# Optimization experiments

Measured on AMD Instinct MI355X. Metric: run time of the kernel, lower is better.

The kernel has to match this reference:

```python
import jax, jax.numpy as jnp
import numpy as np

B, TV, F, H, V, NSTEPS = 64, 40, 2048, 1024, 32000, 30


def setup_inputs() -> dict:
    key = jax.random.key(0)
    ks = jax.random.split(key, 26)
    s = 0.02
    return {
        "batch_size": B,
        "action_feat": jax.random.normal(ks[0], (B, TV, F), jnp.float32),
        "imagenet_feat": jax.random.normal(ks[1], (B, TV, F), jnp.float32),
        "video_mask": jnp.ones((B, TV), jnp.float32),
        "captions": jax.random.randint(ks[2], (B, NSTEPS + 1), 0, V),
        "caption_mask": jnp.ones((B, NSTEPS + 1), jnp.float32),
        "enc_img_W": jax.random.normal(ks[3], (F, H), jnp.float32) * s,
        "enc_img_b": jax.random.normal(ks[4], (H,), jnp.float32) * s,
        "enc_mean_W": jax.random.normal(ks[5], (F, H), jnp.float32) * s,
        "enc_mean_b": jax.random.normal(ks[6], (H,), jnp.float32) * s,
        "att_w": jax.random.normal(ks[7], (H,), jnp.float32) * s,
        "att_Wa": jax.random.normal(ks[8], (H, H), jnp.float32) * s,
        "att_Ua": jax.random.normal(ks[9], (H, H), jnp.float32) * s,
        "att_ba": jax.random.normal(ks[10], (H,), jnp.float32) * s,
        "Wemb": jax.random.normal(ks[11], (V, H), jnp.float32) * s,
        "embed_word_W": jax.random.normal(ks[12], (H, V), jnp.float32) * s,
        "embed_word_b": jax.random.normal(ks[13], (V,), jnp.float32) * s,
        "lstm1_Wih": jax.random.normal(ks[14], (4 * H, 2 * H), jnp.float32) * s,
        "lstm1_Whh": jax.random.normal(ks[15], (4 * H, H), jnp.float32) * s,
        "lstm1_bih": jax.random.normal(ks[16], (4 * H,), jnp.float32) * s,
        "lstm1_bhh": jax.random.normal(ks[17], (4 * H,), jnp.float32) * s,
        "lstm2_Wih": jax.random.normal(ks[18], (4 * H, H), jnp.float32) * s,
        "lstm2_Whh": jax.random.normal(ks[19], (4 * H, H), jnp.float32) * s,
        "lstm2_bih": jax.random.normal(ks[20], (4 * H,), jnp.float32) * s,
        "lstm2_bhh": jax.random.normal(ks[21], (4 * H,), jnp.float32) * s,
    }


def _lstm_cell(x, h, c, Wih, Whh, bih, bhh):
    # PyTorch LSTMCell: gates in order (i, f, g, o)
    g = x @ Wih.T + bih + h @ Whh.T + bhh
    i, f, gg, o = jnp.split(g, 4, axis=-1)
    c_new = jax.nn.sigmoid(f) * c + jax.nn.sigmoid(i) * jnp.tanh(gg)
    h_new = jax.nn.sigmoid(o) * jnp.tanh(c_new)
    return h_new, c_new


def reference(batch_size, action_feat, imagenet_feat, video_mask, captions,
              caption_mask, enc_img_W, enc_img_b, enc_mean_W, enc_mean_b,
              att_w, att_Wa, att_Ua, att_ba, Wemb, embed_word_W, embed_word_b,
              lstm1_Wih, lstm1_Whh, lstm1_bih, lstm1_bhh,
              lstm2_Wih, lstm2_Whh, lstm2_bih, lstm2_bhh):
    bsz = action_feat.shape[0]
    # source code overwrites cat(action, imagenet) with action_feat alone
    video_feat = action_feat @ enc_img_W + enc_img_b          # [B, Tv, H]
    vid_emb = jnp.transpose(video_feat, (1, 0, 2))            # [Tv, B, H]
    feat_mean = jnp.mean(action_feat, axis=1)                 # [B, F]
    feat_mean = feat_mean @ enc_mean_W + enc_mean_b           # [B, H]

    image_part = jnp.einsum('tbh,hk->tbk', vid_emb, att_Ua) + att_ba  # [Tv,B,H]
    vm = video_mask.T                                         # [Tv, B]

    n = captions.shape[1] - 1
    emb_seq = jnp.transpose(Wemb[captions[:, :n]], (1, 0, 2))  # [n, B, H]
    tgts = captions[:, 1:n + 1].T                              # [n, B]
    masks = caption_mask[:, 1:n + 1].T                         # [n, B]

    zeros_h = jnp.zeros((bsz, vid_emb.shape[-1]), jnp.float32)

    def step(carry, xs):
        h1, c1, h2, c2, h_prev, loss = carry
        emb_t, tgt_t, mask_t = xs
        # Bahdanau attention with custom masked softmax
        e = jnp.tanh(h_prev @ att_Wa + image_part)             # [Tv, B, H]
        e = jnp.einsum('tbh,h->tb', e, att_w)                  # [Tv, B]
        e_max = jnp.max(e, axis=0)                             # [B]
        e_hat = vm * jnp.exp(e - e_max)                        # [Tv, B]
        denom = jnp.sum(e_hat, axis=0)
        denom = denom + (denom == 0.0).astype(jnp.float32) + 1e-9
        e_div = e_hat / denom                                  # [Tv, B]
        atten = jnp.einsum('tb,tbh->bh', e_div, vid_emb)       # [B, H]

        x1 = jnp.concatenate([emb_t, atten], axis=1)           # [B, 2H]
        h1, c1 = _lstm_cell(x1, h1, c1, lstm1_Wih, lstm1_Whh, lstm1_bih, lstm1_bhh)
        h2, c2 = _lstm_cell(h1, h2, c2, lstm2_Wih, lstm2_Whh, lstm2_bih, lstm2_bhh)

        logits = h2 @ embed_word_W + embed_word_b              # [B, V]
        logp = jax.nn.log_softmax(logits, axis=-1)
        ce_mean = -jnp.mean(jnp.take_along_axis(logp, tgt_t[:, None], axis=1)[:, 0])
        # original: scalar mean-CE broadcast over mask, summed, / batch_size
        loss = loss + ce_mean * jnp.sum(mask_t) / bsz
        return (h1, c1, h2, c2, h2, loss), None

    init = (feat_mean, zeros_h, zeros_h, zeros_h, feat_mean, jnp.float32(0.0))
    (h1, c1, h2, c2, h_prev, total_loss), _ = jax.lax.scan(
        step, init, (emb_seq, tgts, masks))
    return total_loss
```

## Files before the change

### kernel.cpp

```cpp
#include <hip/hip_runtime.h>
#include <stdint.h>

constexpr int kB   = 64;
constexpr int kTV  = 40;
constexpr int kF   = 2048;
constexpr int kH   = 1024;
constexpr int kV   = 32000;
constexpr int kNS  = 30;
constexpr int kCAP = 31;

typedef __attribute__((ext_vector_type(8))) short bf16x8;
typedef __attribute__((ext_vector_type(4))) float f32x4;
typedef unsigned short us;

__device__ __forceinline__ float sigm(float x) { return 1.f / (1.f + __expf(-x)); }
__device__ __forceinline__ float tanh_fast(float x) {
    float e = __expf(2.f * x);
    return 1.f - 2.f / (e + 1.f);
}
__device__ __forceinline__ us f2bf(float x) {
    unsigned u = __float_as_uint(x);
    return (us)((u + 0x7fffu + ((u >> 16) & 1u)) >> 16);
}
__device__ __forceinline__ float bf2f(us u) {
    return __uint_as_float((unsigned)u << 16);
}

__device__ __forceinline__ void gl16(const us* g, us* lds) {
    __builtin_amdgcn_global_load_lds(
        (const __attribute__((address_space(1))) unsigned int*)(g),
        (__attribute__((address_space(3))) unsigned int*)(lds), 16, 0, 0);
}

template <int N>
__device__ __forceinline__ void waitv() {
    asm volatile("s_waitcnt vmcnt(%0)" :: "n"(N) : "memory");
}
__device__ __forceinline__ void barrier_raw() {
    __builtin_amdgcn_s_barrier();
    asm volatile("" ::: "memory");
}

__device__ __forceinline__ void store_packedA(us* base, int row, int col, us v) {
    int kt = col >> 5, kc = col & 31, ms = row >> 4;
    int l = (row & 15) + (((kc >> 2) & 3) << 4);
    int j = (kc & 3) + ((kc >> 4) << 2);
    base[((((size_t)kt * 4 + ms) * 64 + l) << 3) + j] = v;
}

template <int NSPW, int KT>
__device__ __forceinline__ void mfma_kloop(
    const us* __restrict__ Ap, const us* __restrict__ Bp,
    us* Asm, us* Bsm, int w, int l, f32x4 acc[4][NSPW])
{
    constexpr int BSTEP = 2048 * NSPW;
    constexpr int LPT = 1 + NSPW;
    auto stage = [&](int t, int slot) {
        gl16(Ap + (size_t)t * 2048 + w * 512 + l * 8, Asm + slot * 2048 + w * 512);
#pragma unroll
        for (int i = 0; i < NSPW; ++i)
            gl16(Bp + (size_t)t * BSTEP + (w * NSPW + i) * 512 + l * 8,
                 Bsm + slot * BSTEP + (w * NSPW + i) * 512);
    };
    stage(0, 0);
    if (1 < KT) stage(1, 1);
#pragma unroll 1
    for (int t = 0; t < KT; ++t) {
        int slot = t % 3;
        if (t + 1 < KT) waitv<LPT>();
        else waitv<0>();
        barrier_raw();
        if (t + 2 < KT) stage(t + 2, (t + 2) % 3);
        bf16x8 bfr[NSPW], afr[4];
#pragma unroll
        for (int i = 0; i < NSPW; ++i)
            bfr[i] = *(const bf16x8*)(Bsm + slot * BSTEP + ((w * NSPW + i) * 64 + l) * 8);
#pragma unroll
        for (int ms = 0; ms < 4; ++ms)
            afr[ms] = *(const bf16x8*)(Asm + slot * 2048 + (ms * 64 + l) * 8);
#pragma unroll
        for (int ms = 0; ms < 4; ++ms)
#pragma unroll
            for (int i = 0; i < NSPW; ++i)
                acc[ms][i] = __builtin_amdgcn_mfma_f32_16x16x32_bf16(
                    afr[ms], bfr[i], acc[ms][i], 0, 0, 0);
        __builtin_amdgcn_sched_barrier(0);
    }
}

__global__ __launch_bounds__(256) void prep_mean(
    const float* __restrict__ af, float* __restrict__ fm,
    const float* __restrict__ bih1, const float* __restrict__ bhh1,
    const float* __restrict__ bih2, const float* __restrict__ bhh2,
    const float* __restrict__ capmask,
    float* __restrict__ bsum1, float* __restrict__ bsum2, float* __restrict__ msum)
{
    int tid = threadIdx.x;
    if (blockIdx.x < 64) {
        int b = blockIdx.x;
        const float* base = af + (size_t)b * kTV * kF;
        float a[8] = {};
        for (int t = 0; t < kTV; ++t) {
            const float* rp = base + (size_t)t * kF + tid * 8;
            float4 v0 = *(const float4*)rp;
            float4 v1 = *(const float4*)(rp + 4);
            a[0] += v0.x; a[1] += v0.y; a[2] += v0.z; a[3] += v0.w;
            a[4] += v1.x; a[5] += v1.y; a[6] += v1.z; a[7] += v1.w;
        }
        float* op = fm + (size_t)b * kF + tid * 8;
#pragma unroll
        for (int j = 0; j < 8; ++j) op[j] = a[j] * (1.f / kTV);
    } else {
        int g = (blockIdx.x - 64) * 256 + tid;
        if (g < 4096) bsum1[g] = bih1[g] + bhh1[g];
        else if (g < 8192) { int j = g - 4096; bsum2[j] = bih2[j] + bhh2[j]; }
        else if (g < 8192 + kNS) {
            int t = g - 8192;
            float s = 0.f;
            for (int b = 0; b < kB; ++b) s += capmask[b * kCAP + t + 1];
            msum[t] = s;
        }
    }
}

__global__ __launch_bounds__(256) void pack_rm(
    const float* __restrict__ p0, int ld0, int ksplit,
    const float* __restrict__ p1, int ld1,
    int NGRP, int GS, int HS, int KT,
    us* __restrict__ out)
{
    __shared__ us tile[16][136];
    int kb = blockIdx.x * 128;
    int grp = blockIdx.y;
    int row0 = (grp % NGRP) * GS + (grp / NGRP) * HS;
    int tid = threadIdx.x;
    int r = tid >> 5, c4 = (tid & 31) * 4;
#pragma unroll
    for (int pass = 0; pass < 2; ++pass) {
        int rr = r + pass * 8;
        int row = row0 + rr;
        int k = kb + c4;
        float4 v;
        if (k < ksplit) v = *(const float4*)(p0 + (size_t)row * ld0 + k);
        else            v = *(const float4*)(p1 + (size_t)row * ld1 + (k - ksplit));
        ushort4 o; o.x = f2bf(v.x); o.y = f2bf(v.y); o.z = f2bf(v.z); o.w = f2bf(v.w);
        *(ushort4*)&tile[rr][c4] = o;
    }
    __syncthreads();
    int ktl = tid >> 6, l = tid & 63, ul = l & 15, q = (l >> 4) & 3;
    __align__(16) us o2[8];
#pragma unroll
    for (int j = 0; j < 8; ++j) {
        int kc = (j & 3) + q * 4 + ((j >> 2) << 4);
        o2[j] = tile[ul][ktl * 32 + kc];
    }
    int kt = (kb >> 5) + ktl;
    size_t base = (((size_t)(grp / NGRP) * KT + kt) * NGRP + (grp % NGRP)) * 512;
    *(uint4*)(out + base + (size_t)l * 8) = *(const uint4*)o2;
}

__global__ __launch_bounds__(256) void pack_cm(const float* __restrict__ W,
                                               us* __restrict__ out)
{
    __shared__ us tile[32][136];
    int n0 = blockIdx.x * 128, k0 = blockIdx.y * 32;
    int tid = threadIdx.x;
    int r = tid >> 5, c4 = (tid & 31) * 4;
#pragma unroll
    for (int pass = 0; pass < 4; ++pass) {
        int rr = r + pass * 8;
        float4 v = *(const float4*)(W + (size_t)(k0 + rr) * kV + n0 + c4);
        ushort4 o; o.x = f2bf(v.x); o.y = f2bf(v.y); o.z = f2bf(v.z); o.w = f2bf(v.w);
        *(ushort4*)&tile[rr][c4] = o;
    }
    __syncthreads();
    int ns = tid >> 5, lp = (tid & 31) * 2;
    size_t base = (((size_t)blockIdx.x * 32 + blockIdx.y) * 8 + ns) * 512;
    __align__(16) us o2[16];
#pragma unroll
    for (int li = 0; li < 2; ++li) {
        int l = lp + li, ul = l & 15, q = (l >> 4) & 3;
#pragma unroll
        for (int j = 0; j < 8; ++j) {
            int kc = (j & 3) + q * 4 + ((j >> 2) << 4);
            o2[li * 8 + j] = tile[kc][ns * 16 + ul];
        }
    }
    *(uint4*)(out + base + lp * 8) = *(const uint4*)&o2[0];
    *(uint4*)(out + base + lp * 8 + 8) = *(const uint4*)&o2[8];
}

__global__ __launch_bounds__(256) void pack_sm4(
    const float* __restrict__ Wi, const float* __restrict__ Wm,
    const float* __restrict__ Wua, const float* __restrict__ Wa,
    us* __restrict__ oi, us* __restrict__ om,
    us* __restrict__ oua, us* __restrict__ oa)
{
    int bid = blockIdx.x;
    const float* W; us* out; int KT, rel;
    if (bid < 512)       { W = Wi;  out = oi;  KT = 64; rel = bid; }
    else if (bid < 1024) { W = Wm;  out = om;  KT = 64; rel = bid - 512; }
    else if (bid < 1280) { W = Wua; out = oua; KT = 32; rel = bid - 1024; }
    else                 { W = Wa;  out = oa;  KT = 32; rel = bid - 1280; }
    int bx = rel & 7, by = rel >> 3;
    __shared__ us tile[32][136];
    int n0 = bx * 128, k0 = by * 32;
    int tid = threadIdx.x;
    int r = tid >> 5, c4 = (tid & 31) * 4;
#pragma unroll
    for (int pass = 0; pass < 4; ++pass) {
        int rr = r + pass * 8;
        float4 v = *(const float4*)(W + (size_t)(k0 + rr) * 1024 + n0 + c4);
        ushort4 o; o.x = f2bf(v.x); o.y = f2bf(v.y); o.z = f2bf(v.z); o.w = f2bf(v.w);
        *(ushort4*)&tile[rr][c4] = o;
    }
    __syncthreads();
    int ns = tid >> 5, lp = (tid & 31) * 2;
    int nb64 = bx * 2 + (ns >> 2), ns4 = ns & 3;
    size_t base = (((size_t)nb64 * KT + by) * 4 + ns4) * 512;
    __align__(16) us o2[16];
#pragma unroll
    for (int li = 0; li < 2; ++li) {
        int l = lp + li, ul = l & 15, q = (l >> 4) & 3;
#pragma unroll
        for (int j = 0; j < 8; ++j) {
            int kc = (j & 3) + q * 4 + ((j >> 2) << 4);
            o2[li * 8 + j] = tile[kc][ns * 16 + ul];
        }
    }
    *(uint4*)(out + base + lp * 8) = *(const uint4*)&o2[0];
    *(uint4*)(out + base + lp * 8 + 8) = *(const uint4*)&o2[8];
}

__global__ __launch_bounds__(256) void pack_wae(const float* __restrict__ Wa,
                                                us* __restrict__ WaE)
{
    int nb = blockIdx.x >> 4, cb = blockIdx.x & 15;
    int tid = threadIdx.x;
    int ns = tid >> 6, l = tid & 63;
    int ul = l & 15, q = (l >> 4) & 3;
    int col = cb * 64 + ns * 16 + ul;
    __align__(16) us o[8];
#pragma unroll
    for (int j = 0; j < 4; ++j) {
        int k = (j & 3) + q * 4;
        o[j] = f2bf(Wa[(size_t)(nb * 16 + k) * kH + col]);
    }
    o[4] = 0; o[5] = 0; o[6] = 0; o[7] = 0;
    size_t base = (((size_t)(nb * 16 + cb)) * 4 + ns) * 512;
    *(uint4*)(WaE + base + (size_t)l * 8) = *(const uint4*)o;
}

__global__ __launch_bounds__(256) void pack_emb(
    const float* __restrict__ Wemb, const int* __restrict__ captions,
    us* __restrict__ embP)
{
    __shared__ us tile[16][136];
    int rel = blockIdx.x;
    int s = rel / 32, rem = rel % 32;
    int rg = rem & 3, kb8 = rem >> 2;
    int tid = threadIdx.x;
    int r = tid >> 5, c4 = (tid & 31) * 4;
#pragma unroll
    for (int pass = 0; pass < 2; ++pass) {
        int rr = r + pass * 8;
        int b = rg * 16 + rr;
        int word = captions[b * kCAP + s];
        float4 v = *(const float4*)(Wemb + (size_t)word * kH + kb8 * 128 + c4);
        ushort4 o; o.x = f2bf(v.x); o.y = f2bf(v.y); o.z = f2bf(v.z); o.w = f2bf(v.w);
        *(ushort4*)&tile[rr][c4] = o;
    }
    __syncthreads();
    int ktl = tid >> 6, l = tid & 63, ul = l & 15, q = (l >> 4) & 3;
    __align__(16) us o2[8];
#pragma unroll
    for (int j = 0; j < 8; ++j) {
        int kc = (j & 3) + q * 4 + ((j >> 2) << 4);
        o2[j] = tile[ul][ktl * 32 + kc];
    }
    int kt = kb8 * 4 + ktl;
    size_t base = (((size_t)s * 32 + kt) * 4 + rg) * 512;
    *(uint4*)(embP + base + (size_t)l * 8) = *(const uint4*)o2;
}

template <int KT>
__global__ __launch_bounds__(256) void enc_gemm(
    const us* __restrict__ Ap, const us* __restrict__ Bp,
    const float* __restrict__ bias, us* __restrict__ outF,
    us* __restrict__ outP)
{
    __shared__ us Asm[3][2048];
    __shared__ us Bsm[3][2048];
    int tid = threadIdx.x, w = tid >> 6, l = tid & 63;
    int nb = blockIdx.x, mb = blockIdx.y;
    f32x4 acc[4][1] = {};
    mfma_kloop<1, KT>(Ap + (size_t)mb * KT * 2048, Bp + (size_t)nb * KT * 2048,
                      &Asm[0][0], &Bsm[0][0], w, l, acc);
    int ul = l & 15, sg = l >> 4;
    int n = nb * 64 + w * 16 + ul;
    float bv = bias[n];
#pragma unroll
    for (int ms = 0; ms < 4; ++ms)
#pragma unroll
        for (int r = 0; r < 4; ++r) {
            int rl = ms * 16 + sg * 4 + r;
            int row = mb * 64 + rl;
            float v = acc[ms][0][r] + bv;
            outF[(size_t)row * kH + n] = f2bf(v);
            if (outP) store_packedA(outP + (size_t)mb * 65536, rl, n, f2bf(v));
        }
}

__global__ __launch_bounds__(256) void p3_gemm(
    const us* __restrict__ Ap, const us* __restrict__ Bp,
    const float* __restrict__ bias, us* __restrict__ xcat1p,
    us* __restrict__ h2hist0)
{
    __shared__ us Asm[3][2048];
    __shared__ us Bsm[3][2048];
    int tid = threadIdx.x, w = tid >> 6, l = tid & 63;
    int nb = blockIdx.x;
    f32x4 acc[4][1] = {};
    mfma_kloop<1, 64>(Ap, Bp + (size_t)nb * 64 * 2048, &Asm[0][0], &Bsm[0][0], w, l, acc);
    int ul = l & 15, sg = l >> 4;
    int n = nb * 64 + w * 16 + ul;
    float bv = bias[n];
#pragma unroll
    for (int ms = 0; ms < 4; ++ms)
#pragma unroll
        for (int r = 0; r < 4; ++r) {
            int row = ms * 16 + sg * 4 + r;
            us hb = f2bf(acc[ms][0][r] + bv);
            store_packedA(xcat1p, row, 1024 + n, hb);
            store_packedA(h2hist0, row, n, hb);
        }
}

__global__ __launch_bounds__(256) void gemb_gemm(
    const us* __restrict__ embP, const us* __restrict__ W1p,
    us* __restrict__ Gemb)
{
    __shared__ us Asm[3][2048];
    __shared__ us Bsm[3][2048];
    int rel = blockIdx.x;
    int s = rel >> 6, nb = rel & 63;
    int tid = threadIdx.x, w = tid >> 6, l = tid & 63;
    f32x4 acc[4][1] = {};
    mfma_kloop<1, 32>(embP + (size_t)s * 65536, W1p + (size_t)nb * 96 * 2048,
                      &Asm[0][0], &Bsm[0][0], w, l, acc);
    int ul = l & 15, sg = l >> 4;
    int n = nb * 64 + w * 16 + ul;
#pragma unroll
    for (int ms = 0; ms < 4; ++ms)
#pragma unroll
        for (int r = 0; r < 4; ++r) {
            int row = ms * 16 + sg * 4 + r;
            Gemb[((size_t)s * 64 + row) * 4096 + n] = f2bf(acc[ms][0][r]);
        }
}

__global__ __launch_bounds__(512) void hwa_gemm(
    const us* __restrict__ h2p, const us* __restrict__ WaP,
    float* __restrict__ hw)
{
    __shared__ __align__(16) char smem[49152];
    float* rsum = (float*)smem;
    int tid = threadIdx.x, w = tid >> 6, l = tid & 63, nb = blockIdx.x;
    int h = w >> 2, w4 = w & 3;
    us* Asm = (us*)(smem + h * 24576);
    us* Bsm = Asm + 6144;
    f32x4 acc[4][1] = {};
    mfma_kloop<1, 16>(h2p + (size_t)h * 16 * 2048,
                      WaP + (size_t)nb * 32 * 2048 + (size_t)h * 16 * 2048,
                      Asm, Bsm, w4, l, acc);
    int ul = l & 15, sg = l >> 4;
    __syncthreads();
    if (h == 1) {
#pragma unroll
        for (int ms = 0; ms < 4; ++ms)
#pragma unroll
            for (int r = 0; r < 4; ++r)
                rsum[((w4 * 64) + ms * 16 + sg * 4 + r) * 17 + ul] = acc[ms][0][r];
    }
    __syncthreads();
    if (h == 0) {
        int n = nb * 64 + w4 * 16 + ul;
#pragma unroll
        for (int ms = 0; ms < 4; ++ms)
#pragma unroll
            for (int r = 0; r < 4; ++r) {
                int row = ms * 16 + sg * 4 + r;
                hw[(size_t)row * kH + n] =
                    acc[ms][0][r] + rsum[((w4 * 64) + row) * 17 + ul];
            }
    }
}

__global__ __launch_bounds__(256) void attn_fused(
    const float* __restrict__ hw0, const us* __restrict__ hwP,
    const us* __restrict__ imgp, const float* __restrict__ attw,
    const us* __restrict__ vf, const float* __restrict__ vmask,
    us* __restrict__ xcat1p)
{
    __shared__ float hwv[kH];
    __shared__ float es[48];
    int b = blockIdx.x, tid = threadIdx.x;
    if (hw0) {
        for (int i = tid; i < kH; i += 256) hwv[i] = hw0[(size_t)b * kH + i];
    } else {
        int c4 = tid * 4;
        float a0 = 0.f, a1 = 0.f, a2 = 0.f, a3 = 0.f;
        for (int nb = 0; nb < 64; ++nb) {
            ushort4 v = *(const ushort4*)(hwP + ((size_t)nb * 64 + b) * 1024 + c4);
            a0 += bf2f(v.x); a1 += bf2f(v.y); a2 += bf2f(v.z); a3 += bf2f(v.w);
        }
        hwv[c4 + 0] = a0; hwv[c4 + 1] = a1; hwv[c4 + 2] = a2; hwv[c4 + 3] = a3;
    }
    __syncthreads();
    int w = tid >> 6, l = tid & 63;
    for (int t = w; t < kTV; t += 4) {
        const us* ip = imgp + ((size_t)b * kTV + t) * kH;
        float p = 0.f;
#pragma unroll
        for (int hh = 0; hh < 16; ++hh) {
            int h = hh * 64 + l;
            p += tanh_fast(hwv[h] + bf2f(ip[h])) * attw[h];
        }
        for (int off = 32; off; off >>= 1) p += __shfl_down(p, off);
        if (l == 0) es[t] = p;
    }
    __syncthreads();
    float mx = -1e30f;
    for (int t = 0; t < kTV; ++t) mx = fmaxf(mx, es[t]);
    const float* vm = vmask + b * kTV;
    float den = 0.f;
    for (int t = 0; t < kTV; ++t) den += vm[t] * __expf(es[t] - mx);
    den = den + (den == 0.f ? 1.f : 0.f) + 1e-9f;
    int h0 = tid * 4;
    float a0 = 0.f, a1 = 0.f, a2 = 0.f, a3 = 0.f;
    for (int t = 0; t < kTV; ++t) {
        float wgt = vm[t] * __expf(es[t] - mx) / den;
        ushort4 v = *(const ushort4*)(vf + ((size_t)b * kTV + t) * kH + h0);
        a0 += wgt * bf2f(v.x); a1 += wgt * bf2f(v.y);
        a2 += wgt * bf2f(v.z); a3 += wgt * bf2f(v.w);
    }
    store_packedA(xcat1p, b, h0 + 0, f2bf(a0));
    store_packedA(xcat1p, b, h0 + 1, f2bf(a1));
    store_packedA(xcat1p, b, h0 + 2, f2bf(a2));
    store_packedA(xcat1p, b, h0 + 3, f2bf(a3));
}

template <int KT, int BSTR, int KOFF>
__global__ __launch_bounds__(1024) void gates_cell(
    const us* __restrict__ Ap, const us* __restrict__ Bp,
    const float* __restrict__ bsum, const us* __restrict__ gemb,
    float* __restrict__ cbuf,
    us* __restrict__ dA, int ofsA, us* __restrict__ dB, int ofsB)
{
    __shared__ __align__(16) char smem[98304];
    float* gsm = (float*)smem;
    constexpr int KQ = KT / 4;
    int tid = threadIdx.x, w16 = tid >> 6, l = tid & 63, nb = blockIdx.x;
    int g = w16 >> 2, w4 = w16 & 3;
    us* Asm = (us*)(smem + g * 24576);
    us* Bsm = Asm + 6144;
    f32x4 acc[4][1] = {};
    mfma_kloop<1, KQ>(Ap + (size_t)g * KQ * 2048,
                      Bp + (size_t)nb * BSTR * 2048 + (size_t)(KOFF + g * KQ) * 2048,
                      Asm, Bsm, w4, l, acc);
    int ul = l & 15, sg = l >> 4;
    int sl = (g & 1) * 4 + w4;
    float bv = (g == 0) ? bsum[w4 * 1024 + nb * 16 + ul] : 0.f;
    __syncthreads();
    if (g < 2) {
#pragma unroll
        for (int ms = 0; ms < 4; ++ms)
#pragma unroll
            for (int r = 0; r < 4; ++r)
                gsm[(sl * 64 + ms * 16 + sg * 4 + r) * 17 + ul] = acc[ms][0][r] + bv;
    }
    __syncthreads();
    if (g >= 2) {
#pragma unroll
        for (int ms = 0; ms < 4; ++ms)
#pragma unroll
            for (int r = 0; r < 4; ++r)
                gsm[(sl * 64 + ms * 16 + sg * 4 + r) * 17 + ul] += acc[ms][0][r];
    }
    __syncthreads();
    {
        int row = tid >> 4, uc = tid & 15, u = nb * 16 + uc;
        float ge0 = 0.f, ge1 = 0.f, ge2 = 0.f, ge3 = 0.f;
        if (gemb) {
            const us* gp = gemb + (size_t)row * 4096 + nb * 64 + uc;
            ge0 = bf2f(gp[0]); ge1 = bf2f(gp[16]);
            ge2 = bf2f(gp[32]); ge3 = bf2f(gp[48]);
        }
        float gi = gsm[((0 * 64) + row) * 17 + uc] + gsm[((4 * 64) + row) * 17 + uc] + ge0;
        float gf = gsm[((1 * 64) + row) * 17 + uc] + gsm[((5 * 64) + row) * 17 + uc] + ge1;
        float gg = gsm[((2 * 64) + row) * 17 + uc] + gsm[((6 * 64) + row) * 17 + uc] + ge2;
        float go = gsm[((3 * 64) + row) * 17 + uc] + gsm[((7 * 64) + row) * 17 + uc] + ge3;
        float c = sigm(gf) * cbuf[(size_t)row * kH + u] + sigm(gi) * tanh_fast(gg);
        cbuf[(size_t)row * kH + u] = c;
        us hb = f2bf(sigm(go) * tanh_fast(c));
        store_packedA(dA, row, ofsA + u, hb);
        store_packedA(dB, row, ofsB + u, hb);
    }
}

__global__ __launch_bounds__(1024) void gates2_cell(
    const us* __restrict__ Ap, const us* __restrict__ Bp,
    const float* __restrict__ bsum, float* __restrict__ cbuf,
    us* __restrict__ dA, int ofsA, us* __restrict__ dB, int ofsB,
    us* __restrict__ hwPart, const us* __restrict__ WaE)
{
    __shared__ __align__(16) char smem[98304];
    float* gsm = (float*)smem;
    us* hA = (us*)(smem + 40960);
    constexpr int KQ = 16;
    int tid = threadIdx.x, w16 = tid >> 6, l = tid & 63, nb = blockIdx.x;
    int g = w16 >> 2, w4 = w16 & 3;
    us* Asm = (us*)(smem + g * 24576);
    us* Bsm = Asm + 6144;
    f32x4 acc[4][1] = {};
    mfma_kloop<1, KQ>(Ap + (size_t)g * KQ * 2048,
                      Bp + (size_t)nb * 64 * 2048 + (size_t)(g * KQ) * 2048,
                      Asm, Bsm, w4, l, acc);
    int ul = l & 15, sg = l >> 4;
    int sl = (g & 1) * 4 + w4;
    float bv = (g == 0) ? bsum[w4 * 1024 + nb * 16 + ul] : 0.f;
    __syncthreads();
    if (g < 2) {
#pragma unroll
        for (int ms = 0; ms < 4; ++ms)
#pragma unroll
            for (int r = 0; r < 4; ++r)
                gsm[(sl * 64 + ms * 16 + sg * 4 + r) * 17 + ul] = acc[ms][0][r] + bv;
    }
    __syncthreads();
    if (g >= 2) {
#pragma unroll
        for (int ms = 0; ms < 4; ++ms)
#pragma unroll
            for (int r = 0; r < 4; ++r)
                gsm[(sl * 64 + ms * 16 + sg * 4 + r) * 17 + ul] += acc[ms][0][r];
    }
    __syncthreads();
    int row = tid >> 4, uc = tid & 15, u = nb * 16 + uc;
    {
        float gi = gsm[((0 * 64) + row) * 17 + uc] + gsm[((4 * 64) + row) * 17 + uc];
        float gf = gsm[((1 * 64) + row) * 17 + uc] + gsm[((5 * 64) + row) * 17 + uc];
        float gg = gsm[((2 * 64) + row) * 17 + uc] + gsm[((6 * 64) + row) * 17 + uc];
        float go = gsm[((3 * 64) + row) * 17 + uc] + gsm[((7 * 64) + row) * 17 + uc];
        float c = sigm(gf) * cbuf[(size_t)row * kH + u] + sigm(gi) * tanh_fast(gg);
        cbuf[(size_t)row * kH + u] = c;
        us hb = f2bf(sigm(go) * tanh_fast(c));
        store_packedA(dA, row, ofsA + u, hb);
        store_packedA(dB, row, ofsB + u, hb);
        if (hwPart) {
            *(unsigned*)(hA + tid * 2) = 0;
            __syncthreads();
            int lpos = (row & 15) + (((uc >> 2) & 3) << 4);
            hA[((((row >> 4) * 64) + lpos) << 3) + (uc & 3)] = hb;
            __syncthreads();
            int cb = w16;
            f32x4 hacc[4][4] = {};
            bf16x8 afr[4];
#pragma unroll
            for (int ms = 0; ms < 4; ++ms)
                afr[ms] = *(const bf16x8*)(hA + (ms * 64 + l) * 8);
#pragma unroll
            for (int ns = 0; ns < 4; ++ns) {
                bf16x8 bfr = *(const bf16x8*)(WaE +
                    ((((size_t)(nb * 16 + cb)) * 4 + ns) << 9) + l * 8);
#pragma unroll
                for (int ms = 0; ms < 4; ++ms)
                    hacc[ms][ns] = __builtin_amdgcn_mfma_f32_16x16x32_bf16(
                        afr[ms], bfr, hacc[ms][ns], 0, 0, 0);
            }
#pragma unroll
            for (int ms = 0; ms < 4; ++ms)
#pragma unroll
                for (int ns = 0; ns < 4; ++ns)
#pragma unroll
                    for (int r = 0; r < 4; ++r) {
                        int row2 = ms * 16 + sg * 4 + r;
                        int col = cb * 64 + ns * 16 + ul;
                        hwPart[((size_t)nb * 64 + row2) * 1024 + col] =
                            f2bf(hacc[ms][ns][r]);
                    }
        }
    }
}

__global__ __launch_bounds__(256) void logits_sb(
    const us* __restrict__ h2hist, const us* __restrict__ WvP,
    const float* __restrict__ embb, const int* __restrict__ captions,
    float* __restrict__ psumP, float* __restrict__ tlogs)
{
    constexpr int SBLK = 3;
    __shared__ us Asm[SBLK][3][2048];
    __shared__ us Bsm[3][4096];
    __shared__ float rsum[4][64];
    __shared__ int stgt[SBLK][64];
    int bid = blockIdx.x;
    int c = bid & 7, q = bid >> 3;
    int sgrp = q % 10, nb = c + (q / 10) * 8;
    if (nb >= 250) return;
    int s0 = sgrp * SBLK;
    int tid = threadIdx.x, w = tid >> 6, l = tid & 63, ul = l & 15, lsg = l >> 4;
    if (tid < 64)
#pragma unroll
        for (int si = 0; si < SBLK; ++si)
            stgt[si][tid] = captions[tid * kCAP + s0 + si + 1];
    const us* Ab0 = h2hist + (size_t)(s0 + 1) * 65536;
    const us* Ab1 = h2hist + (size_t)(s0 + 2) * 65536;
    const us* Ab2 = h2hist + (size_t)(s0 + 3) * 65536;
    const us* Bb  = WvP + (size_t)nb * 32 * 4096;
    auto stage = [&](int t, int slot) {
        gl16(Ab0 + (size_t)t * 2048 + w * 512 + l * 8, &Asm[0][slot][w * 512]);
        gl16(Ab1 + (size_t)t * 2048 + w * 512 + l * 8, &Asm[1][slot][w * 512]);
        gl16(Ab2 + (size_t)t * 2048 + w * 512 + l * 8, &Asm[2][slot][w * 512]);
#pragma unroll
        for (int i = 0; i < 2; ++i)
            gl16(Bb + (size_t)t * 4096 + (w * 2 + i) * 512 + l * 8,
                 &Bsm[slot][(w * 2 + i) * 512]);
    };
    f32x4 acc[SBLK][4][2] = {};
    stage(0, 0); stage(1, 1);
#pragma unroll 1
    for (int t = 0; t < 32; ++t) {
        int slot = t % 3;
        if (t + 1 < 32) waitv<5>();
        else waitv<0>();
        barrier_raw();
        if (t + 2 < 32) stage(t + 2, (t + 2) % 3);
        bf16x8 b0 = *(const bf16x8*)&Bsm[slot][((w * 2 + 0) * 64 + l) * 8];
        bf16x8 b1 = *(const bf16x8*)&Bsm[slot][((w * 2 + 1) * 64 + l) * 8];
#pragma unroll
        for (int ms = 0; ms < 4; ++ms)
#pragma unroll
            for (int si = 0; si < SBLK; ++si) {
                bf16x8 a = *(const bf16x8*)&Asm[si][slot][(ms * 64 + l) * 8];
                acc[si][ms][0] = __builtin_amdgcn_mfma_f32_16x16x32_bf16(
                    a, b0, acc[si][ms][0], 0, 0, 0);
                acc[si][ms][1] = __builtin_amdgcn_mfma_f32_16x16x32_bf16(
                    a, b1, acc[si][ms][1], 0, 0, 0);
            }
        __builtin_amdgcn_sched_barrier(0);
    }
    int n0 = nb * 128 + (2 * w + 0) * 16 + ul;
    int n1 = nb * 128 + (2 * w + 1) * 16 + ul;
    float e0 = embb[n0], e1 = embb[n1];
#pragma unroll
    for (int si = 0; si < SBLK; ++si) {
        float ls[4][4];
#pragma unroll
        for (int ms = 0; ms < 4; ++ms)
#pragma unroll
            for (int r = 0; r < 4; ++r) {
                int row = ms * 16 + lsg * 4 + r;
                float v0 = acc[si][ms][0][r] + e0, v1 = acc[si][ms][1][r] + e1;
                ls[ms][r] = __expf(v0) + __expf(v1);
                if (n0 == stgt[si][row]) tlogs[(s0 + si) * 64 + row] = v0;
                if (n1 == stgt[si][row]) tlogs[(s0 + si) * 64 + row] = v1;
            }
#pragma unroll
        for (int m = 1; m < 16; m <<= 1)
#pragma unroll
            for (int ms = 0; ms < 4; ++ms)
#pragma unroll
                for (int r = 0; r < 4; ++r)
                    ls[ms][r] += __shfl_xor(ls[ms][r], m);
        if (ul == 0)
#pragma unroll
            for (int ms = 0; ms < 4; ++ms)
#pragma unroll
                for (int r = 0; r < 4; ++r)
                    rsum[w][ms * 16 + lsg * 4 + r] = ls[ms][r];
        __syncthreads();
        if (tid < 64)
            psumP[((size_t)(s0 + si) * 250 + nb) * 64 + tid] =
                rsum[0][tid] + rsum[1][tid] + rsum[2][tid] + rsum[3][tid];
        __syncthreads();
    }
}

__global__ __launch_bounds__(256) void final_loss(
    const float* __restrict__ psumP, const float* __restrict__ tlogs,
    const float* __restrict__ msum, float* __restrict__ out)
{
    __shared__ float sl[16000];
    int s = blockIdx.x, tid = threadIdx.x;
    const float* src = psumP + (size_t)s * 16000;
    for (int i = tid; i < 16000; i += 256) sl[i] = src[i];
    __syncthreads();
    if (tid < 64) {
        float tot = 0.f;
        for (int i = 0; i < 250; ++i) tot += sl[i * 64 + tid];
        float logp = tlogs[s * 64 + tid] - __logf(tot);
        float term = -logp * msum[s] * (1.f / 4096.f);
        for (int off = 32; off; off >>= 1) term += __shfl_down(term, off);
        if (tid == 0) atomicAdd(out, term);
    }
}

extern "C" void kernel_launch(void* const* d_in, const int* in_sizes, int n_in,
                              void* d_out, int out_size, void* d_ws, size_t ws_size,
                              hipStream_t stream)
{
    const float* action_feat = (const float*)d_in[1];
    const float* video_mask  = (const float*)d_in[3];
    const int*   captions    = (const int*)d_in[4];
    const float* capmask     = (const float*)d_in[5];
    const float* enc_img_W   = (const float*)d_in[6];
    const float* enc_img_b   = (const float*)d_in[7];
    const float* enc_mean_W  = (const float*)d_in[8];
    const float* enc_mean_b  = (const float*)d_in[9];
    const float* att_w       = (const float*)d_in[10];
    const float* att_Wa      = (const float*)d_in[11];
    const float* att_Ua      = (const float*)d_in[12];
    const float* att_ba      = (const float*)d_in[13];
    const float* Wemb        = (const float*)d_in[14];
    const float* embW        = (const float*)d_in[15];
    const float* embb        = (const float*)d_in[16];
    const float* W1ih        = (const float*)d_in[17];
    const float* W1hh        = (const float*)d_in[18];
    const float* b1ih        = (const float*)d_in[19];
    const float* b1hh        = (const float*)d_in[20];
    const float* W2ih        = (const float*)d_in[21];
    const float* W2hh        = (const float*)d_in[22];
    const float* b2ih        = (const float*)d_in[23];
    const float* b2hh        = (const float*)d_in[24];

    char* base = (char*)d_ws;
    size_t off = 0;
    auto alloc = [&](size_t bytes) {
        char* p = base + off;
        off = (off + bytes + 255) & ~(size_t)255;
        return p;
    };
    constexpr int BIG = 0x40000000;

    us* vf       = (us*)alloc((size_t)2560 * 1024 * 2);
    us* imgp     = (us*)alloc((size_t)2560 * 1024 * 2);
    float* fm    = (float*)alloc((size_t)64 * 2048 * 4);
    float* hw    = (float*)alloc((size_t)64 * 1024 * 4);
    us* hwPart   = (us*)alloc((size_t)64 * 64 * 1024 * 2);
    float* bsum1 = (float*)alloc(4096 * 4);
    float* bsum2 = (float*)alloc(4096 * 4);
    float* msum  = (float*)alloc(32 * 4);
    float* psumP = (float*)alloc((size_t)kNS * 250 * 64 * 4);
    float* tlogs = (float*)alloc((size_t)kNS * 64 * 4);
    us* Gemb     = (us*)alloc((size_t)kNS * 64 * 4096 * 2);
    us* x2p0 = (us*)alloc((size_t)64 * 2048 * 2);
    us* x2p1 = (us*)alloc((size_t)64 * 2048 * 2);
    float* c1    = (float*)alloc((size_t)64 * 1024 * 4);
    float* c2    = (float*)alloc((size_t)64 * 1024 * 4);
    size_t zlen  = (size_t)((char*)(c2 + 64 * 1024) - (char*)x2p0);

    us* x1p0 = (us*)alloc((size_t)64 * 2048 * 2);
    us* x1p1 = (us*)alloc((size_t)64 * 2048 * 2);
    us* h2hist = (us*)alloc((size_t)(kNS + 1) * 64 * 1024 * 2);
    us* embP = (us*)alloc((size_t)kNS * 64 * 1024 * 2);
    us* afP  = (us*)alloc((size_t)2560 * 2048 * 2);
    us* vfP  = (us*)alloc((size_t)2560 * 1024 * 2);
    us* fmP  = (us*)alloc((size_t)64 * 2048 * 2);
    us* WiP  = (us*)alloc((size_t)2048 * 1024 * 2);
    us* WmP  = (us*)alloc((size_t)2048 * 1024 * 2);
    us* WuaP = (us*)alloc((size_t)1024 * 1024 * 2);
    us* WaP  = (us*)alloc((size_t)1024 * 1024 * 2);
    us* WaE  = (us*)alloc((size_t)64 * 16 * 4 * 512 * 2);
    us* W1p  = (us*)alloc((size_t)3072 * 4096 * 2);
    us* W2p  = (us*)alloc((size_t)2048 * 4096 * 2);
    us* WvP  = (us*)alloc((size_t)1024 * 32000 * 2);
    if (off > ws_size) return;

    hipMemsetAsync(d_out, 0, 4, stream);
    hipMemsetAsync(x2p0, 0, zlen, stream);

    prep_mean<<<97, 256, 0, stream>>>(action_feat, fm, b1ih, b1hh, b2ih, b2hh,
                                      capmask, bsum1, bsum2, msum);
    pack_rm<<<dim3(16, 4), 256, 0, stream>>>(fm, 2048, BIG, nullptr, 0,
                                             4, 16, 64, 64, fmP);
    pack_rm<<<dim3(16, 160), 256, 0, stream>>>(action_feat, 2048, BIG, nullptr, 0,
                                               4, 16, 64, 64, afP);
    pack_rm<<<dim3(24, 256), 256, 0, stream>>>(W1ih, 2048, 2048, W1hh, 1024,
                                               4, 1024, 16, 96, W1p);
    pack_rm<<<dim3(16, 256), 256, 0, stream>>>(W2ih, 1024, 1024, W2hh, 1024,
                                               4, 1024, 16, 64, W2p);
    pack_sm4<<<1536, 256, 0, stream>>>(enc_img_W, enc_mean_W, att_Ua, att_Wa,
                                       WiP, WmP, WuaP, WaP);
    pack_wae<<<1024, 256, 0, stream>>>(att_Wa, WaE);
    pack_cm<<<dim3(250, 32), 256, 0, stream>>>(embW, WvP);
    pack_emb<<<960, 256, 0, stream>>>(Wemb, captions, embP);

    enc_gemm<64><<<dim3(16, 40), 256, 0, stream>>>(afP, WiP, enc_img_b, vf, vfP);
    p3_gemm<<<16, 256, 0, stream>>>(fmP, WmP, enc_mean_b, x1p0, h2hist);
    enc_gemm<32><<<dim3(16, 40), 256, 0, stream>>>(vfP, WuaP, att_ba, imgp, nullptr);
    gemb_gemm<<<1920, 256, 0, stream>>>(embP, W1p, Gemb);
    hwa_gemm<<<16, 512, 0, stream>>>(h2hist, WaP, hw);

    for (int s = 0; s < kNS; ++s) {
        us* x1c = (s & 1) ? x1p1 : x1p0;
        us* x1n = (s & 1) ? x1p0 : x1p1;
        us* x2c = (s & 1) ? x2p1 : x2p0;
        us* x2n = (s & 1) ? x2p0 : x2p1;
        attn_fused<<<64, 256, 0, stream>>>(
            (s == 0) ? hw : nullptr, hwPart, imgp, att_w, vf, video_mask, x1c);
        gates_cell<64, 96, 32><<<64, 1024, 0, stream>>>(
            x1c, W1p, bsum1, Gemb + (size_t)s * 64 * 4096, c1,
            x1n, 1024, x2c, 0);
        gates2_cell<<<64, 1024, 0, stream>>>(
            x2c, W2p, bsum2, c2,
            x2n, 1024, h2hist + (size_t)(s + 1) * 65536, 0,
            (s < kNS - 1) ? hwPart : nullptr, WaE);
    }
    logits_sb<<<2560, 256, 0, stream>>>(h2hist, WvP, embb, captions, psumP, tlogs);
    final_loss<<<kNS, 256, 0, stream>>>(psumP, tlogs, msum, (float*)d_out);
}
```

Measured before the change: 1.883 ms.

## Overlap vocabulary logits work with recurrent steps by piggybacking on attention launches

```diff
diff --git a/kernel.cpp b/kernel.cpp
--- a/kernel.cpp
+++ b/kernel.cpp
@@ -396,15 +396,110 @@
     }
 }
 
-__global__ __launch_bounds__(256) void attn_fused(
+__global__ __launch_bounds__(256) void attn_logits(
     const float* __restrict__ hw0, const us* __restrict__ hwP,
     const us* __restrict__ imgp, const float* __restrict__ attw,
     const us* __restrict__ vf, const float* __restrict__ vmask,
-    us* __restrict__ xcat1p)
-{
-    __shared__ float hwv[kH];
-    __shared__ float es[48];
-    int b = blockIdx.x, tid = threadIdx.x;
+    us* __restrict__ xcat1p,
+    const us* __restrict__ h2hist, const us* __restrict__ WvP,
+    const float* __restrict__ embb, const int* __restrict__ captions,
+    float* __restrict__ psumP, float* __restrict__ tlogs, int lgStart)
+{
+    __shared__ __align__(16) char smem[63488];
+    int tid = threadIdx.x, w = tid >> 6, l = tid & 63, ul = l & 15, lsg = l >> 4;
+    if (blockIdx.x >= 64) {
+        us* Asm = (us*)smem;
+        us* Bsm = (us*)(smem + 36864);
+        float* rsum = (float*)(smem + 61440);
+        int* stgt = (int*)(smem + 62464);
+        int lb = lgStart + (int)blockIdx.x - 64;
+        int g = lb / 250, nb = lb % 250;
+        int s0 = g * 3;
+        if (tid < 64)
+#pragma unroll
+            for (int si = 0; si < 3; ++si)
+                stgt[si * 64 + tid] = captions[tid * kCAP + s0 + si + 1];
+        const us* Ab0 = h2hist + (size_t)(s0 + 1) * 65536;
+        const us* Ab1 = h2hist + (size_t)(s0 + 2) * 65536;
+        const us* Ab2 = h2hist + (size_t)(s0 + 3) * 65536;
+        const us* Bb  = WvP + (size_t)nb * 32 * 4096;
+        auto stage = [&](int t, int slot) {
+            gl16(Ab0 + (size_t)t * 2048 + w * 512 + l * 8,
+                 Asm + (0 * 3 + slot) * 2048 + w * 512);
+            gl16(Ab1 + (size_t)t * 2048 + w * 512 + l * 8,
+                 Asm + (1 * 3 + slot) * 2048 + w * 512);
+            gl16(Ab2 + (size_t)t * 2048 + w * 512 + l * 8,
+                 Asm + (2 * 3 + slot) * 2048 + w * 512);
+#pragma unroll
+            for (int i = 0; i < 2; ++i)
+                gl16(Bb + (size_t)t * 4096 + (w * 2 + i) * 512 + l * 8,
+                     Bsm + slot * 4096 + (w * 2 + i) * 512);
+        };
+        f32x4 acc[3][4][2] = {};
+        stage(0, 0); stage(1, 1);
+#pragma unroll 1
+        for (int t = 0; t < 32; ++t) {
+            int slot = t % 3;
+            if (t + 1 < 32) waitv<5>();
+            else waitv<0>();
+            barrier_raw();
+            if (t + 2 < 32) stage(t + 2, (t + 2) % 3);
+            bf16x8 b0 = *(const bf16x8*)(Bsm + slot * 4096 + ((w * 2 + 0) * 64 + l) * 8);
+            bf16x8 b1 = *(const bf16x8*)(Bsm + slot * 4096 + ((w * 2 + 1) * 64 + l) * 8);
+#pragma unroll
+            for (int ms = 0; ms < 4; ++ms)
+#pragma unroll
+                for (int si = 0; si < 3; ++si) {
+                    bf16x8 a = *(const bf16x8*)(Asm + (si * 3 + slot) * 2048 +
+                                                (ms * 64 + l) * 8);
+                    acc[si][ms][0] = __builtin_amdgcn_mfma_f32_16x16x32_bf16(
+                        a, b0, acc[si][ms][0], 0, 0, 0);
+                    acc[si][ms][1] = __builtin_amdgcn_mfma_f32_16x16x32_bf16(
+                        a, b1, acc[si][ms][1], 0, 0, 0);
+                }
+            __builtin_amdgcn_sched_barrier(0);
+        }
+        int n0 = nb * 128 + (2 * w + 0) * 16 + ul;
+        int n1 = nb * 128 + (2 * w + 1) * 16 + ul;
+        float e0 = embb[n0], e1 = embb[n1];
+#pragma unroll
+        for (int si = 0; si < 3; ++si) {
+            float ls[4][4];
+#pragma unroll
+            for (int ms = 0; ms < 4; ++ms)
+#pragma unroll
+                for (int r = 0; r < 4; ++r) {
+                    int row = ms * 16 + lsg * 4 + r;
+                    float v0 = acc[si][ms][0][r] + e0, v1 = acc[si][ms][1][r] + e1;
+                    ls[ms][r] = __expf(v0) + __expf(v1);
+                    if (n0 == stgt[si * 64 + row]) tlogs[(s0 + si) * 64 + row] = v0;
+                    if (n1 == stgt[si * 64 + row]) tlogs[(s0 + si) * 64 + row] = v1;
+                }
+#pragma unroll
+            for (int m = 1; m < 16; m <<= 1)
+#pragma unroll
+                for (int ms = 0; ms < 4; ++ms)
+#pragma unroll
+                    for (int r = 0; r < 4; ++r)
+                        ls[ms][r] += __shfl_xor(ls[ms][r], m);
+            if (ul == 0)
+#pragma unroll
+                for (int ms = 0; ms < 4; ++ms)
+#pragma unroll
+                    for (int r = 0; r < 4; ++r)
+                        rsum[w * 64 + ms * 16 + lsg * 4 + r] = ls[ms][r];
+            __syncthreads();
+            if (tid < 64)
+                psumP[((size_t)(s0 + si) * 250 + nb) * 64 + tid] =
+                    rsum[0 * 64 + tid] + rsum[1 * 64 + tid] +
+                    rsum[2 * 64 + tid] + rsum[3 * 64 + tid];
+            __syncthreads();
+        }
+        return;
+    }
+    float* hwv = (float*)smem;
+    float* es = (float*)(smem + 4096);
+    int b = blockIdx.x;
     if (hw0) {
         for (int i = tid; i < kH; i += 256) hwv[i] = hw0[(size_t)b * kH + i];
     } else {
@@ -417,7 +512,6 @@
         hwv[c4 + 0] = a0; hwv[c4 + 1] = a1; hwv[c4 + 2] = a2; hwv[c4 + 3] = a3;
     }
     __syncthreads();
-    int w = tid >> 6, l = tid & 63;
     for (int t = w; t < kTV; t += 4) {
         const us* ip = imgp + ((size_t)b * kTV + t) * kH;
         float p = 0.f;
@@ -448,6 +542,96 @@
     store_packedA(xcat1p, b, h0 + 1, f2bf(a1));
     store_packedA(xcat1p, b, h0 + 2, f2bf(a2));
     store_packedA(xcat1p, b, h0 + 3, f2bf(a3));
+}
+
+__global__ __launch_bounds__(256) void logits_tail(
+    const us* __restrict__ h2hist, const us* __restrict__ WvP,
+    const float* __restrict__ embb, const int* __restrict__ captions,
+    float* __restrict__ psumP, float* __restrict__ tlogs, int lgStart)
+{
+    __shared__ us Asm[3][3][2048];
+    __shared__ us Bsm[3][4096];
+    __shared__ float rsum[4][64];
+    __shared__ int stgt[3][64];
+    int lb = lgStart + (int)blockIdx.x;
+    int g = lb / 250, nb = lb % 250;
+    int s0 = g * 3;
+    int tid = threadIdx.x, w = tid >> 6, l = tid & 63, ul = l & 15, lsg = l >> 4;
+    if (tid < 64)
+#pragma unroll
+        for (int si = 0; si < 3; ++si)
+            stgt[si][tid] = captions[tid * kCAP + s0 + si + 1];
+    const us* Ab0 = h2hist + (size_t)(s0 + 1) * 65536;
+    const us* Ab1 = h2hist + (size_t)(s0 + 2) * 65536;
+    const us* Ab2 = h2hist + (size_t)(s0 + 3) * 65536;
+    const us* Bb  = WvP + (size_t)nb * 32 * 4096;
+    auto stage = [&](int t, int slot) {
+        gl16(Ab0 + (size_t)t * 2048 + w * 512 + l * 8, &Asm[0][slot][w * 512]);
+        gl16(Ab1 + (size_t)t * 2048 + w * 512 + l * 8, &Asm[1][slot][w * 512]);
+        gl16(Ab2 + (size_t)t * 2048 + w * 512 + l * 8, &Asm[2][slot][w * 512]);
+#pragma unroll
+        for (int i = 0; i < 2; ++i)
+            gl16(Bb + (size_t)t * 4096 + (w * 2 + i) * 512 + l * 8,
+                 &Bsm[slot][(w * 2 + i) * 512]);
+    };
+    f32x4 acc[3][4][2] = {};
+    stage(0, 0); stage(1, 1);
+#pragma unroll 1
+    for (int t = 0; t < 32; ++t) {
+        int slot = t % 3;
+        if (t + 1 < 32) waitv<5>();
+        else waitv<0>();
+        barrier_raw();
+        if (t + 2 < 32) stage(t + 2, (t + 2) % 3);
+        bf16x8 b0 = *(const bf16x8*)&Bsm[slot][((w * 2 + 0) * 64 + l) * 8];
+        bf16x8 b1 = *(const bf16x8*)&Bsm[slot][((w * 2 + 1) * 64 + l) * 8];
+#pragma unroll
+        for (int ms = 0; ms < 4; ++ms)
+#pragma unroll
+            for (int si = 0; si < 3; ++si) {
+                bf16x8 a = *(const bf16x8*)&Asm[si][slot][(ms * 64 + l) * 8];
+                acc[si][ms][0] = __builtin_amdgcn_mfma_f32_16x16x32_bf16(
+                    a, b0, acc[si][ms][0], 0, 0, 0);
+                acc[si][ms][1] = __builtin_amdgcn_mfma_f32_16x16x32_bf16(
+                    a, b1, acc[si][ms][1], 0, 0, 0);
+            }
+        __builtin_amdgcn_sched_barrier(0);
+    }
+    int n0 = nb * 128 + (2 * w + 0) * 16 + ul;
+    int n1 = nb * 128 + (2 * w + 1) * 16 + ul;
+    float e0 = embb[n0], e1 = embb[n1];
+#pragma unroll
+    for (int si = 0; si < 3; ++si) {
+        float ls[4][4];
+#pragma unroll
+        for (int ms = 0; ms < 4; ++ms)
+#pragma unroll
+            for (int r = 0; r < 4; ++r) {
+                int row = ms * 16 + lsg * 4 + r;
+                float v0 = acc[si][ms][0][r] + e0, v1 = acc[si][ms][1][r] + e1;
+                ls[ms][r] = __expf(v0) + __expf(v1);
+                if (n0 == stgt[si][row]) tlogs[(s0 + si) * 64 + row] = v0;
+                if (n1 == stgt[si][row]) tlogs[(s0 + si) * 64 + row] = v1;
+            }
+#pragma unroll
+        for (int m = 1; m < 16; m <<= 1)
+#pragma unroll
+            for (int ms = 0; ms < 4; ++ms)
+#pragma unroll
+                for (int r = 0; r < 4; ++r)
+                    ls[ms][r] += __shfl_xor(ls[ms][r], m);
+        if (ul == 0)
+#pragma unroll
+            for (int ms = 0; ms < 4; ++ms)
+#pragma unroll
+                for (int r = 0; r < 4; ++r)
+                    rsum[w][ms * 16 + lsg * 4 + r] = ls[ms][r];
+        __syncthreads();
+        if (tid < 64)
+            psumP[((size_t)(s0 + si) * 250 + nb) * 64 + tid] =
+                rsum[0][tid] + rsum[1][tid] + rsum[2][tid] + rsum[3][tid];
+        __syncthreads();
+    }
 }
 
 template <int KT, int BSTR, int KOFF>
@@ -590,99 +774,6 @@
                             f2bf(hacc[ms][ns][r]);
                     }
         }
-    }
-}
-
-__global__ __launch_bounds__(256) void logits_sb(
-    const us* __restrict__ h2hist, const us* __restrict__ WvP,
-    const float* __restrict__ embb, const int* __restrict__ captions,
-    float* __restrict__ psumP, float* __restrict__ tlogs)
-{
-    constexpr int SBLK = 3;
-    __shared__ us Asm[SBLK][3][2048];
-    __shared__ us Bsm[3][4096];
-    __shared__ float rsum[4][64];
-    __shared__ int stgt[SBLK][64];
-    int bid = blockIdx.x;
-    int c = bid & 7, q = bid >> 3;
-    int sgrp = q % 10, nb = c + (q / 10) * 8;
-    if (nb >= 250) return;
-    int s0 = sgrp * SBLK;
-    int tid = threadIdx.x, w = tid >> 6, l = tid & 63, ul = l & 15, lsg = l >> 4;
-    if (tid < 64)
-#pragma unroll
-        for (int si = 0; si < SBLK; ++si)
-            stgt[si][tid] = captions[tid * kCAP + s0 + si + 1];
-    const us* Ab0 = h2hist + (size_t)(s0 + 1) * 65536;
-    const us* Ab1 = h2hist + (size_t)(s0 + 2) * 65536;
-    const us* Ab2 = h2hist + (size_t)(s0 + 3) * 65536;
-    const us* Bb  = WvP + (size_t)nb * 32 * 4096;
-    auto stage = [&](int t, int slot) {
-        gl16(Ab0 + (size_t)t * 2048 + w * 512 + l * 8, &Asm[0][slot][w * 512]);
-        gl16(Ab1 + (size_t)t * 2048 + w * 512 + l * 8, &Asm[1][slot][w * 512]);
-        gl16(Ab2 + (size_t)t * 2048 + w * 512 + l * 8, &Asm[2][slot][w * 512]);
-#pragma unroll
-        for (int i = 0; i < 2; ++i)
-            gl16(Bb + (size_t)t * 4096 + (w * 2 + i) * 512 + l * 8,
-                 &Bsm[slot][(w * 2 + i) * 512]);
-    };
-    f32x4 acc[SBLK][4][2] = {};
-    stage(0, 0); stage(1, 1);
-#pragma unroll 1
-    for (int t = 0; t < 32; ++t) {
-        int slot = t % 3;
-        if (t + 1 < 32) waitv<5>();
-        else waitv<0>();
-        barrier_raw();
-        if (t + 2 < 32) stage(t + 2, (t + 2) % 3);
-        bf16x8 b0 = *(const bf16x8*)&Bsm[slot][((w * 2 + 0) * 64 + l) * 8];
-        bf16x8 b1 = *(const bf16x8*)&Bsm[slot][((w * 2 + 1) * 64 + l) * 8];
-#pragma unroll
-        for (int ms = 0; ms < 4; ++ms)
-#pragma unroll
-            for (int si = 0; si < SBLK; ++si) {
-                bf16x8 a = *(const bf16x8*)&Asm[si][slot][(ms * 64 + l) * 8];
-                acc[si][ms][0] = __builtin_amdgcn_mfma_f32_16x16x32_bf16(
-                    a, b0, acc[si][ms][0], 0, 0, 0);
-                acc[si][ms][1] = __builtin_amdgcn_mfma_f32_16x16x32_bf16(
-                    a, b1, acc[si][ms][1], 0, 0, 0);
-            }
-        __builtin_amdgcn_sched_barrier(0);
-    }
-    int n0 = nb * 128 + (2 * w + 0) * 16 + ul;
-    int n1 = nb * 128 + (2 * w + 1) * 16 + ul;
-    float e0 = embb[n0], e1 = embb[n1];
-#pragma unroll
-    for (int si = 0; si < SBLK; ++si) {
-        float ls[4][4];
-#pragma unroll
-        for (int ms = 0; ms < 4; ++ms)
-#pragma unroll
-            for (int r = 0; r < 4; ++r) {
-                int row = ms * 16 + lsg * 4 + r;
-                float v0 = acc[si][ms][0][r] + e0, v1 = acc[si][ms][1][r] + e1;
-                ls[ms][r] = __expf(v0) + __expf(v1);
-                if (n0 == stgt[si][row]) tlogs[(s0 + si) * 64 + row] = v0;
-                if (n1 == stgt[si][row]) tlogs[(s0 + si) * 64 + row] = v1;
-            }
-#pragma unroll
-        for (int m = 1; m < 16; m <<= 1)
-#pragma unroll
-            for (int ms = 0; ms < 4; ++ms)
-#pragma unroll
-                for (int r = 0; r < 4; ++r)
-                    ls[ms][r] += __shfl_xor(ls[ms][r], m);
-        if (ul == 0)
-#pragma unroll
-            for (int ms = 0; ms < 4; ++ms)
-#pragma unroll
-                for (int r = 0; r < 4; ++r)
-                    rsum[w][ms * 16 + lsg * 4 + r] = ls[ms][r];
-        __syncthreads();
-        if (tid < 64)
-            psumP[((size_t)(s0 + si) * 250 + nb) * 64 + tid] =
-                rsum[0][tid] + rsum[1][tid] + rsum[2][tid] + rsum[3][tid];
-        __syncthreads();
     }
 }
 
@@ -801,13 +892,20 @@
     gemb_gemm<<<1920, 256, 0, stream>>>(embP, W1p, Gemb);
     hwa_gemm<<<16, 512, 0, stream>>>(h2hist, WaP, hw);
 
+    int issued = 0;
     for (int s = 0; s < kNS; ++s) {
         us* x1c = (s & 1) ? x1p1 : x1p0;
         us* x1n = (s & 1) ? x1p0 : x1p1;
         us* x2c = (s & 1) ? x2p1 : x2p0;
         us* x2n = (s & 1) ? x2p0 : x2p1;
-        attn_fused<<<64, 256, 0, stream>>>(
-            (s == 0) ? hw : nullptr, hwPart, imgp, att_w, vf, video_mask, x1c);
+        int ready = (s >= 3) ? 250 * ((s - 3) / 3 + 1) : 0;
+        int cnt = ready - issued;
+        if (cnt > 84) cnt = 84;
+        if (cnt < 0) cnt = 0;
+        attn_logits<<<64 + cnt, 256, 0, stream>>>(
+            (s == 0) ? hw : nullptr, hwPart, imgp, att_w, vf, video_mask, x1c,
+            h2hist, WvP, embb, captions, psumP, tlogs, issued - 0 + (cnt ? 0 : 0));
+        issued += cnt;
         gates_cell<64, 96, 32><<<64, 1024, 0, stream>>>(
             x1c, W1p, bsum1, Gemb + (size_t)s * 64 * 4096, c1,
             x1n, 1024, x2c, 0);
@@ -816,6 +914,8 @@
             x2n, 1024, h2hist + (size_t)(s + 1) * 65536, 0,
             (s < kNS - 1) ? hwPart : nullptr, WaE);
     }
-    logits_sb<<<2560, 256, 0, stream>>>(h2hist, WvP, embb, captions, psumP, tlogs);
+    int rem = 2500 - issued;
+    logits_tail<<<rem, 256, 0, stream>>>(h2hist, WvP, embb, captions,
+                                         psumP, tlogs, issued);
     final_loss<<<kNS, 256, 0, stream>>>(psumP, tlogs, msum, (float*)d_out);
 }
```

Measured after the change: 1.807 ms. -4.0%, faster.
